# Kernel tuning notes

Hardware: AMD Instinct MI355X
Metric: run time of the kernel (lower is better)

## Reference

```python
import jax, jax.numpy as jnp
import numpy as np

HIDDEN = 2048
NUM_HEADS = 16
HEAD_DIM = 128
ROPE_BASE = 10000.0
B, L = 2, 2048


def _rotate_half(x):
    x1, x2 = jnp.split(x, 2, axis=-1)
    return jnp.concatenate((-x2, x1), axis=-1)


def _apply_rope(x, position_ids, base=ROPE_BASE):
    # x: [B, L, H, D]; position_ids: [L] (broadcast over batch)
    D = x.shape[-1]
    dim_idx = jnp.arange(0, D, 2, dtype=jnp.float32)
    inv_freq = 1.0 / (base ** (dim_idx / D))                      # [D/2]
    freqs = position_ids.astype(jnp.float32)[None, :, None] * inv_freq  # [1, L, D/2]
    # NOTE: faithful to source: sin/cos are repeat_interleaved ([s0,s0,s1,s1,...])
    sin = jnp.repeat(jnp.sin(freqs), 2, axis=-1)[:, :, None, :]   # [1, L, 1, D]
    cos = jnp.repeat(jnp.cos(freqs), 2, axis=-1)[:, :, None, :]
    return cos * x + _rotate_half(x) * sin


def setup_inputs() -> dict:
    key = jax.random.key(0)
    k1, k2, k3, k4, k5 = jax.random.split(key, 5)
    hidden_states = jax.random.normal(k1, (B, L, HIDDEN), dtype=jnp.float32)
    # causal additive mask, broadcastable over heads
    causal = jnp.tril(jnp.ones((L, L), dtype=bool))
    attention_mask = jnp.where(causal, 0.0, -1e9).astype(jnp.float32)
    attention_mask = jnp.broadcast_to(attention_mask, (B, 1, L, L))
    position_ids = jnp.arange(L, dtype=jnp.int64)
    s = 1.0 / np.sqrt(HIDDEN)
    Wq = jax.random.normal(k2, (HIDDEN, NUM_HEADS * HEAD_DIM), dtype=jnp.float32) * s
    Wk = jax.random.normal(k3, (HIDDEN, NUM_HEADS * HEAD_DIM), dtype=jnp.float32) * s
    Wv = jax.random.normal(k4, (HIDDEN, NUM_HEADS * HEAD_DIM), dtype=jnp.float32) * s
    Wo = jax.random.normal(k5, (NUM_HEADS * HEAD_DIM, HIDDEN), dtype=jnp.float32) * s
    return {"hidden_states": hidden_states, "attention_mask": attention_mask,
            "position_ids": position_ids, "Wq": Wq, "Wk": Wk, "Wv": Wv, "Wo": Wo}


def reference(hidden_states, attention_mask, position_ids, Wq, Wk, Wv, Wo):
    Bb, Ll, _ = hidden_states.shape
    H, D = NUM_HEADS, HEAD_DIM
    scale = D ** -0.5
    q = (hidden_states @ Wq).reshape(Bb, Ll, H, D)
    k = (hidden_states @ Wk).reshape(Bb, Ll, H, D)
    v = (hidden_states @ Wv).reshape(Bb, Ll, H, D)
    q = _apply_rope(q, position_ids)
    k = _apply_rope(k, position_ids)
    # [B, H, Lq, Lk]
    scores = jnp.einsum('bqhd,bkhd->bhqk', q, k) * scale + attention_mask
    attn = jax.nn.softmax(scores.astype(jnp.float32), axis=-1).astype(q.dtype)
    out = jnp.einsum('bhqk,bkhd->bqhd', attn, v).reshape(Bb, Ll, H * D)
    return out @ Wo
```

## Files before the change

kernel.cpp:

```cpp
#include <hip/hip_runtime.h>
#include <stdint.h>

typedef uint16_t u16;
typedef __attribute__((ext_vector_type(4))) float f32x4;
typedef __attribute__((ext_vector_type(4))) unsigned short u16x4;
typedef __attribute__((ext_vector_type(8))) __bf16 bf16x8;

#define HIDDEN 2048
#define LSEQ   2048
#define NH     16
#define HD     128
#define NQK    6144
#define QSCALE 0.12751743f
#define M0 32.0f

__device__ __forceinline__ u16 f2b(float f) {
  union { float f; uint32_t u; } v; v.f = f;
  uint32_t r = v.u + 0x7fffu + ((v.u >> 16) & 1u);
  return (u16)(r >> 16);
}
__device__ __forceinline__ float b2f(u16 h) {
  union { uint32_t u; float f; } v; v.u = ((uint32_t)h) << 16;
  return v.f;
}

__device__ __forceinline__ void gload16(const void* g, void* l) {
  __builtin_amdgcn_global_load_lds((const __attribute__((address_space(1))) void*)g,
                                   (__attribute__((address_space(3))) void*)l, 16, 0, 0);
}
__device__ __forceinline__ f32x4 mfma16(bf16x8 a, bf16x8 b, f32x4 c) {
  return __builtin_amdgcn_mfma_f32_16x16x32_bf16(a, b, c, 0, 0, 0);
}

__global__ void k_f32_to_bf16(const float* __restrict__ in, u16* __restrict__ out, int n4) {
  int i = blockIdx.x * 256 + threadIdx.x;
  if (i >= n4) return;
  float4 v = ((const float4*)in)[i];
  u16x4 o = { f2b(v.x), f2b(v.y), f2b(v.z), f2b(v.w) };
  ((u16x4*)out)[i] = o;
}

__global__ __launch_bounds__(256) void k_transpose_bf16(const float* __restrict__ W,
                                                        u16* __restrict__ WT, int R, int C,
                                                        float scale, int perm) {
  __shared__ u16 tile[64][65];
  const int bx = blockIdx.x, by = blockIdx.y;
  const int t = threadIdx.x;
  const int g = t >> 4, k = t & 15;
#pragma unroll
  for (int p = 0; p < 4; ++p) {
    int r = by * 64 + p * 16 + g;
    int c = bx * 64 + k * 4;
    float4 v = *(const float4*)(W + (size_t)r * C + c);
    tile[p * 16 + g][k * 4 + 0] = f2b(v.x * scale);
    tile[p * 16 + g][k * 4 + 1] = f2b(v.y * scale);
    tile[p * 16 + g][k * 4 + 2] = f2b(v.z * scale);
    tile[p * 16 + g][k * 4 + 3] = f2b(v.w * scale);
  }
  __syncthreads();
#pragma unroll
  for (int p = 0; p < 4; ++p) {
    int n = bx * 64 + p * 16 + g;
    if (perm) n = (n & ~127) | ((n & 63) << 1) | ((n >> 6) & 1);
    int kk = by * 64 + k * 4;
    u16x4 o = { tile[k * 4 + 0][p * 16 + g], tile[k * 4 + 1][p * 16 + g],
                tile[k * 4 + 2][p * 16 + g], tile[k * 4 + 3][p * 16 + g] };
    *(u16x4*)(WT + (size_t)n * R + kk) = o;
  }
}

__global__ __launch_bounds__(256) void k_transpose_v(const u16* __restrict__ qkv,
                                                     u16* __restrict__ vt) {
  __shared__ u16 tile[64][65];
  const int lt = blockIdx.x;
  const int dt = blockIdx.y;
  const int bh = blockIdx.z;
  const int t = threadIdx.x;
  const int g = t >> 4, k = t & 15;
  const u16* src = qkv + (size_t)(bh >> 4) * LSEQ * NQK + 2 * HIDDEN + (bh & 15) * HD;
#pragma unroll
  for (int p = 0; p < 4; ++p) {
    int l = lt * 64 + p * 16 + g;
    int d = dt * 64 + k * 4;
    u16x4 v = *(const u16x4*)(src + (size_t)l * NQK + d);
    tile[p * 16 + g][k * 4 + 0] = v[0];
    tile[p * 16 + g][k * 4 + 1] = v[1];
    tile[p * 16 + g][k * 4 + 2] = v[2];
    tile[p * 16 + g][k * 4 + 3] = v[3];
  }
  __syncthreads();
  u16* dst = vt + (size_t)bh * HD * LSEQ;
#pragma unroll
  for (int p = 0; p < 4; ++p) {
    int d = dt * 64 + p * 16 + g;
    int l = lt * 64 + k * 4;
    u16x4 o = { tile[k * 4 + 0][p * 16 + g], tile[k * 4 + 1][p * 16 + g],
                tile[k * 4 + 2][p * 16 + g], tile[k * 4 + 3][p * 16 + g] };
    *(u16x4*)(dst + (size_t)d * LSEQ + l) = o;
  }
}

__global__ void k_rope_table(const int* __restrict__ pos, float* __restrict__ tab, int pstride) {
  int i = blockIdx.x * 256 + threadIdx.x;
  int l = i >> 6, j = i & 63;
  float p = (float)pos[(size_t)l * pstride];
  float th = p * expf(-(float)j * 0.14391156642178528f);
  tab[2 * i + 0] = cosf(th);
  tab[2 * i + 1] = sinf(th);
}

template<int BF16OUT, int DOROPE>
__global__ __launch_bounds__(512, 2) void k_gemm2(const u16* __restrict__ A,
                                                  const u16* __restrict__ Bt,
                                                  void* __restrict__ Cv,
                                                  const float* __restrict__ tab,
                                                  int M, int N, int K) {
  __shared__ __align__(16) char lds[147456];
  const int tid = threadIdx.x, w = tid >> 6, lane = tid & 63;
  const int l15 = lane & 15, l4 = lane >> 4;
  const int wm = w >> 2, wn = w & 3;
  const int nbn = gridDim.x, nbm = gridDim.y;
  const int id = blockIdx.y * nbn + blockIdx.x;
  const int x = id & 7, k = id >> 3;
  const int g = nbm >> 3;
  const int bm = x * g + (k % g);
  const int bn = k / g;
  const u16* Ag = A + (size_t)bm * 128 * K;
  const u16* Bg = Bt + (size_t)bn * 256 * K;
  const int r7 = (tid >> 3) & 7;
  const int sw0 = ((0 + l4) ^ (l15 & 7)) * 16;
  const int sw1 = ((4 + l4) ^ (l15 & 7)) * 16;

  auto stageA = [&](int kt, int buf) {
    char* dst = lds + buf * 16384;
    const int k0 = kt << 6;
#pragma unroll
    for (int i = 0; i < 2; ++i) {
      int c = i * 512 + tid;
      int row = c >> 3, s = (c & 7) ^ r7;
      gload16(Ag + (size_t)row * K + k0 + s * 8, dst + (i * 512 + w * 64) * 16);
    }
  };
  auto stageBh = [&](int kt, int buf, int half) {
    char* dst = lds + 49152 + buf * 32768;
    const int k0 = kt << 6;
#pragma unroll
    for (int i = 0; i < 2; ++i) {
      int c = half * 1024 + i * 512 + tid;
      int row = c >> 3, s = (c & 7) ^ r7;
      gload16(Bg + (size_t)row * K + k0 + s * 8, dst + (half * 1024 + i * 512 + w * 64) * 16);
    }
  };

  const int NT = K >> 6;
  stageA(0, 0); stageBh(0, 0, 0); stageBh(0, 0, 1);
  stageA(1, 1); stageBh(1, 1, 0); stageBh(1, 1, 1);
  asm volatile("s_waitcnt vmcnt(6)" ::: "memory");
  __builtin_amdgcn_s_barrier();
  asm volatile("" ::: "memory");

  f32x4 acc[4][4] = {};
  int buf = 0, sbuf = 2;
  for (int t = 0; t < NT; ++t) {
    const char* Ab = lds + buf * 16384;
    const char* Bb = lds + 49152 + buf * 32768;
    const bool doStage = (t + 2 < NT);
    bf16x8 af[4][2], bfr[4][2];
    auto rdA = [&](int mi, int ks) {
      return *(const bf16x8*)(Ab + ((wm * 64 + mi * 16 + l15) << 7) + (ks ? sw1 : sw0));
    };
    auto rdB = [&](int nj, int ks) {
      return *(const bf16x8*)(Bb + ((wn * 64 + nj * 16 + l15) << 7) + (ks ? sw1 : sw0));
    };

#pragma unroll
    for (int mi = 0; mi < 2; ++mi) { af[mi][0] = rdA(mi, 0); af[mi][1] = rdA(mi, 1); }
#pragma unroll
    for (int nj = 0; nj < 2; ++nj) { bfr[nj][0] = rdB(nj, 0); bfr[nj][1] = rdB(nj, 1); }
    if (doStage) stageA(t + 2, sbuf);
    __builtin_amdgcn_s_setprio(1);
#pragma unroll
    for (int mi = 0; mi < 2; ++mi)
#pragma unroll
      for (int nj = 0; nj < 2; ++nj) {
        acc[mi][nj] = mfma16(af[mi][0], bfr[nj][0], acc[mi][nj]);
        acc[mi][nj] = mfma16(af[mi][1], bfr[nj][1], acc[mi][nj]);
      }
    __builtin_amdgcn_s_setprio(0);

#pragma unroll
    for (int nj = 2; nj < 4; ++nj) { bfr[nj][0] = rdB(nj, 0); bfr[nj][1] = rdB(nj, 1); }
    if (doStage) stageBh(t + 2, sbuf, 0);
    __builtin_amdgcn_s_setprio(1);
#pragma unroll
    for (int mi = 0; mi < 2; ++mi)
#pragma unroll
      for (int nj = 2; nj < 4; ++nj) {
        acc[mi][nj] = mfma16(af[mi][0], bfr[nj][0], acc[mi][nj]);
        acc[mi][nj] = mfma16(af[mi][1], bfr[nj][1], acc[mi][nj]);
      }
    __builtin_amdgcn_s_setprio(0);

#pragma unroll
    for (int mi = 2; mi < 4; ++mi) { af[mi][0] = rdA(mi, 0); af[mi][1] = rdA(mi, 1); }
    if (doStage) stageBh(t + 2, sbuf, 1);
    __builtin_amdgcn_s_setprio(1);
#pragma unroll
    for (int mi = 2; mi < 4; ++mi)
#pragma unroll
      for (int nj = 2; nj < 4; ++nj) {
        acc[mi][nj] = mfma16(af[mi][0], bfr[nj][0], acc[mi][nj]);
        acc[mi][nj] = mfma16(af[mi][1], bfr[nj][1], acc[mi][nj]);
      }
    __builtin_amdgcn_s_setprio(0);

    __builtin_amdgcn_s_setprio(1);
#pragma unroll
    for (int mi = 2; mi < 4; ++mi)
#pragma unroll
      for (int nj = 0; nj < 2; ++nj) {
        acc[mi][nj] = mfma16(af[mi][0], bfr[nj][0], acc[mi][nj]);
        acc[mi][nj] = mfma16(af[mi][1], bfr[nj][1], acc[mi][nj]);
      }
    __builtin_amdgcn_s_setprio(0);

    if (doStage) asm volatile("s_waitcnt vmcnt(6)" ::: "memory");
    else         asm volatile("s_waitcnt vmcnt(0)" ::: "memory");
    __builtin_amdgcn_s_barrier();
    asm volatile("" ::: "memory");
    buf = (buf == 2) ? 0 : buf + 1;
    sbuf = (sbuf == 2) ? 0 : sbuf + 1;
  }

  const float2* tb = (const float2*)tab;
#pragma unroll
  for (int mi = 0; mi < 4; ++mi) {
#pragma unroll
    for (int nj = 0; nj < 4; ++nj) {
      int row0 = bm * 128 + wm * 64 + mi * 16 + l4 * 4;
      int col  = bn * 256 + wn * 64 + nj * 16 + l15;
#pragma unroll
      for (int r = 0; r < 4; ++r) {
        float v = acc[mi][nj][r];
        if (DOROPE) {
          float vp = __shfl_xor(v, 1);
          if (col < 4096) {
            int l = (row0 + r) & (LSEQ - 1);
            float2 tt = tb[l * 64 + ((col & 127) >> 2) + ((l15 & 1) << 5)];
            v = (l15 & 1) ? (tt.x * v + tt.y * vp) : (tt.x * v - tt.y * vp);
          }
        }
        if (BF16OUT) ((u16*)Cv)[(size_t)(row0 + r) * N + col] = f2b(v);
        else         ((float*)Cv)[(size_t)(row0 + r) * N + col] = v;
      }
    }
  }
}

__global__ __launch_bounds__(512, 2) void k_attn(const u16* __restrict__ qkv,
                                                 const u16* __restrict__ vt,
                                                 u16* __restrict__ aout) {
  __shared__ __align__(16) u16 Ks[3][64 * 128];
  __shared__ __align__(16) u16 Vs[3][128 * 64];
  __shared__ __align__(16) u16 Ps[2][8 * 16 * 72];
  const int bid = blockIdx.x;
  const int bh = bid & 31, pairi = bid >> 5;
  const int b = bh >> 4, h = bh & 15;
  const int qtA = pairi, qtB = 15 - pairi;
  const int tid = threadIdx.x, w = tid >> 6, lane = tid & 63;
  const int l15 = lane & 15, l4 = lane >> 4;

  bf16x8 qfA[4], qfB[4];
  {
    const u16* qpA = qkv + (size_t)(b * LSEQ + qtA * 128 + w * 16 + l15) * NQK + h * HD;
    const u16* qpB = qkv + (size_t)(b * LSEQ + qtB * 128 + w * 16 + l15) * NQK + h * HD;
#pragma unroll
    for (int ks = 0; ks < 4; ++ks) {
      qfA[ks] = *(const bf16x8*)(qpA + ks * 32 + l4 * 8);
      qfB[ks] = *(const bf16x8*)(qpB + ks * 32 + l4 * 8);
    }
  }

  f32x4 accA[8] = {}, accB[8] = {};
  float mA[4], lA[4], mB[4], lB[4];
#pragma unroll
  for (int r = 0; r < 4; ++r) { mA[r] = M0; lA[r] = 0.f; mB[r] = M0; lB[r] = 0.f; }

  const u16* kb  = qkv + (size_t)b * LSEQ * NQK + HIDDEN + h * HD;
  const u16* vtb = vt + (size_t)bh * HD * LSEQ;
  const int ntA = 2 * qtA + 2, ntB = 2 * qtB + 2;
  const int qbaseA = qtA * 128 + w * 16, qbaseB = qtB * 128 + w * 16;

  auto stage = [&](int t, int bf) {
    const int kv0 = t * 64;
    char* Kd = (char*)(&Ks[bf][0]);
    char* Vd = (char*)(&Vs[bf][0]);
#pragma unroll
    for (int p = 0; p < 2; ++p) {
      int cc = p * 512 + tid;
      int row = cc >> 4, sl = cc & 15;
      gload16(kb + (size_t)(kv0 + row) * NQK + ((sl ^ (row & 7)) * 8), Kd + (p * 512 + w * 64) * 16);
    }
#pragma unroll
    for (int p = 0; p < 2; ++p) {
      int cc = p * 512 + tid;
      int d = cc >> 3, sl = cc & 7;
      gload16(vtb + (size_t)d * LSEQ + kv0 + ((sl ^ (d & 7)) * 8), Vd + (p * 512 + w * 64) * 16);
    }
  };

  auto tileCompute = [&](const bf16x8 (&qf)[4], f32x4 (&acc_o)[8], float (&mrun)[4],
                         float (&lrun)[4], int qbase, int kv0,
                         const char* KsC, const char* VsC, u16* ps) {
    f32x4 s4[4] = {};
    __builtin_amdgcn_s_setprio(1);
#pragma unroll
    for (int ks = 0; ks < 4; ++ks) {
#pragma unroll
      for (int nj = 0; nj < 4; ++nj) {
        int row = nj * 16 + l15;
        int co = (ks * 64 + l4 * 16) ^ ((row & 7) << 4);
        bf16x8 kf = *(const bf16x8*)(KsC + row * 256 + co);
        s4[nj] = mfma16(qf[ks], kf, s4[nj]);
      }
    }
    __builtin_amdgcn_s_setprio(0);

    const int qrow0 = qbase + l4 * 4;
    float pv[4][4], lm[4];
    if (kv0 + 63 <= qbase) {
#pragma unroll
      for (int r = 0; r < 4; ++r) {
        lm[r] = fmaxf(fmaxf(s4[0][r], s4[1][r]), fmaxf(s4[2][r], s4[3][r]));
#pragma unroll
        for (int nj = 0; nj < 4; ++nj) pv[nj][r] = s4[nj][r];
      }
    } else {
#pragma unroll
      for (int r = 0; r < 4; ++r) {
        float mx = -3e38f;
#pragma unroll
        for (int nj = 0; nj < 4; ++nj) {
          int kvcol = kv0 + nj * 16 + l15;
          float sv = (kvcol <= qrow0 + r) ? s4[nj][r] : -3e38f;
          pv[nj][r] = sv;
          mx = fmaxf(mx, sv);
        }
        lm[r] = mx;
      }
    }
    int over = (lm[0] > mrun[0]) | (lm[1] > mrun[1]) | (lm[2] > mrun[2]) | (lm[3] > mrun[3]);
    if (__builtin_expect(__any(over), 0)) {
#pragma unroll
      for (int r = 0; r < 4; ++r) {
        float px = lm[r];
        px = fmaxf(px, __shfl_xor(px, 1));
        px = fmaxf(px, __shfl_xor(px, 2));
        px = fmaxf(px, __shfl_xor(px, 4));
        px = fmaxf(px, __shfl_xor(px, 8));
        if (px > mrun[r]) {
          float cf = exp2f(mrun[r] - px);
          mrun[r] = px;
          lrun[r] *= cf;
#pragma unroll
          for (int df = 0; df < 8; ++df) acc_o[df][r] *= cf;
        }
      }
    }
#pragma unroll
    for (int r = 0; r < 4; ++r) {
      float s = 0.f;
#pragma unroll
      for (int nj = 0; nj < 4; ++nj) {
        float e = exp2f(pv[nj][r] - mrun[r]);
        pv[nj][r] = e;
        s += e;
      }
      lrun[r] += s;
    }
#pragma unroll
    for (int nj = 0; nj < 4; ++nj)
#pragma unroll
      for (int r = 0; r < 4; ++r)
        ps[(w * 16 + l4 * 4 + r) * 72 + nj * 16 + l15] = f2b(pv[nj][r]);

    bf16x8 pa[2];
#pragma unroll
    for (int ks2 = 0; ks2 < 2; ++ks2)
      pa[ks2] = *(const bf16x8*)(ps + (w * 16 + l15) * 72 + ks2 * 32 + l4 * 8);
    __builtin_amdgcn_s_setprio(1);
#pragma unroll
    for (int df = 0; df < 8; ++df) {
#pragma unroll
      for (int ks2 = 0; ks2 < 2; ++ks2) {
        int vrow = df * 16 + l15;
        int co = (ks2 * 64 + l4 * 16) ^ ((vrow & 7) << 4);
        bf16x8 bv = *(const bf16x8*)(VsC + vrow * 128 + co);
        acc_o[df] = mfma16(pa[ks2], bv, acc_o[df]);
      }
    }
    __builtin_amdgcn_s_setprio(0);
  };

  stage(0, 0);
  stage(1, 1);
  asm volatile("s_waitcnt vmcnt(4)" ::: "memory");
  __builtin_amdgcn_s_barrier();

  int buf = 0, sbuf = 2;
  for (int t = 0; t < ntB; ++t) {
    const bool doStage = (t + 2 < ntB);
    if (doStage) stage(t + 2, sbuf);
    const int kv0 = t * 64;
    const char* KsC = (const char*)(&Ks[buf][0]);
    const char* VsC = (const char*)(&Vs[buf][0]);

    if ((t < ntA) && (kv0 <= qbaseA + 15))
      tileCompute(qfA, accA, mA, lA, qbaseA, kv0, KsC, VsC, &Ps[0][0]);
    if (kv0 <= qbaseB + 15)
      tileCompute(qfB, accB, mB, lB, qbaseB, kv0, KsC, VsC, &Ps[1][0]);

    if (doStage) asm volatile("s_waitcnt vmcnt(4)" ::: "memory");
    else         asm volatile("s_waitcnt vmcnt(0)" ::: "memory");
    __builtin_amdgcn_s_barrier();
    buf = (buf == 2) ? 0 : buf + 1;
    sbuf = (sbuf == 2) ? 0 : sbuf + 1;
  }

#pragma unroll
  for (int r = 0; r < 4; ++r) {
    float sA = lA[r];
    sA += __shfl_xor(sA, 1); sA += __shfl_xor(sA, 2);
    sA += __shfl_xor(sA, 4); sA += __shfl_xor(sA, 8);
    float sB = lB[r];
    sB += __shfl_xor(sB, 1); sB += __shfl_xor(sB, 2);
    sB += __shfl_xor(sB, 4); sB += __shfl_xor(sB, 8);
    float invA = 1.f / sA;
    float invB = 1.f / sB;
    u16* opA = aout + (size_t)(b * LSEQ + qtA * 128 + w * 16 + l4 * 4 + r) * HIDDEN + h * HD;
    u16* opB = aout + (size_t)(b * LSEQ + qtB * 128 + w * 16 + l4 * 4 + r) * HIDDEN + h * HD;
#pragma unroll
    for (int df = 0; df < 8; ++df) {
      opA[df * 16 + l15] = f2b(accA[df][r] * invA);
      opB[df * 16 + l15] = f2b(accB[df][r] * invB);
    }
  }
}

extern "C" void kernel_launch(void* const* d_in, const int* in_sizes, int n_in,
                              void* d_out, int out_size, void* d_ws, size_t ws_size,
                              hipStream_t stream) {
  const float* hidden = (const float*)d_in[0];
  const int*   pos = (const int*)d_in[2];
  const float* Wq = (const float*)d_in[3];
  const float* Wk = (const float*)d_in[4];
  const float* Wv = (const float*)d_in[5];
  const float* Wo = (const float*)d_in[6];
  float* out = (float*)d_out;

  char* ws = (char*)d_ws;
  u16* hbf   = (u16*)ws;
  u16* WT    = (u16*)(ws + 16777216);
  u16* vt    = WT;
  u16* WoT   = (u16*)(ws + 16777216 + 25165824);
  u16* qkv   = (u16*)(ws + 50331648);
  float* tab = (float*)(ws + 100663296);
  u16* aout  = hbf;

  int pstride = (in_sizes[2] == LSEQ) ? 1 : 2;

  k_f32_to_bf16<<<8192, 256, 0, stream>>>(hidden, hbf, 2097152);
  dim3 tg(32, 32);
  k_transpose_bf16<<<tg, 256, 0, stream>>>(Wq, WT,                   2048, 2048, QSCALE, 1);
  k_transpose_bf16<<<tg, 256, 0, stream>>>(Wk, WT + 2048 * 2048,     2048, 2048, 1.0f, 1);
  k_transpose_bf16<<<tg, 256, 0, stream>>>(Wv, WT + 2 * 2048 * 2048, 2048, 2048, 1.0f, 0);
  k_transpose_bf16<<<tg, 256, 0, stream>>>(Wo, WoT,                  2048, 2048, 1.0f, 0);
  k_rope_table<<<512, 256, 0, stream>>>(pos, tab, pstride);
  k_gemm2<1, 1><<<dim3(24, 32), 512, 0, stream>>>(hbf, WT, qkv, tab, 4096, 6144, 2048);
  k_transpose_v<<<dim3(32, 2, 32), 256, 0, stream>>>(qkv, vt);
  k_attn<<<256, 512, 0, stream>>>(qkv, vt, aout);
  k_gemm2<0, 0><<<dim3(8, 32), 512, 0, stream>>>(aout, WoT, out, nullptr, 4096, 2048, 2048);
}
```

Measured before the change: 279.9 us.

## Merge weight transposes and rope table into one prep launch; remap GEMM tile order

The four weight transpose/convert launches and the rope-table launch are combined into a single kernel with a z-dimension selecting the job, removing four launch gaps and letting the jobs run concurrently. The GEMM block-to-tile mapping also changes: workgroups are reordered by XCD (id&7) into a contiguous linear tile index with n varying fastest, which changes L2 locality per XCD. The fused kernel adds branching per block, and the z==4 slice launches 1024 blocks where only 512 do work.

```diff
diff --git a/kernel.cpp b/kernel.cpp
--- a/kernel.cpp
+++ b/kernel.cpp
@@ -19,10 +19,6 @@
   uint32_t r = v.u + 0x7fffu + ((v.u >> 16) & 1u);
   return (u16)(r >> 16);
 }
-__device__ __forceinline__ float b2f(u16 h) {
-  union { uint32_t u; float f; } v; v.u = ((uint32_t)h) << 16;
-  return v.f;
-}
 
 __device__ __forceinline__ void gload16(const void* g, void* l) {
   __builtin_amdgcn_global_load_lds((const __attribute__((address_space(1))) void*)g,
@@ -40,9 +36,30 @@
   ((u16x4*)out)[i] = o;
 }
 
-__global__ __launch_bounds__(256) void k_transpose_bf16(const float* __restrict__ W,
-                                                        u16* __restrict__ WT, int R, int C,
-                                                        float scale, int perm) {
+__global__ __launch_bounds__(256) void k_prep(const float* __restrict__ Wq,
+                                              const float* __restrict__ Wk,
+                                              const float* __restrict__ Wv,
+                                              const float* __restrict__ Wo,
+                                              u16* __restrict__ WT, u16* __restrict__ WoT,
+                                              const int* __restrict__ pos, int pstride,
+                                              float* __restrict__ tab) {
+  const int z = blockIdx.z;
+  if (z == 4) {
+    int i = (blockIdx.y * 32 + blockIdx.x) * 256 + threadIdx.x;
+    if (i >= LSEQ * 64) return;
+    int l = i >> 6, j = i & 63;
+    float p = (float)pos[(size_t)l * pstride];
+    float th = p * expf(-(float)j * 0.14391156642178528f);
+    tab[2 * i + 0] = cosf(th);
+    tab[2 * i + 1] = sinf(th);
+    return;
+  }
+  const float* W = (z == 0) ? Wq : (z == 1) ? Wk : (z == 2) ? Wv : Wo;
+  u16* D = (z < 3) ? (WT + (size_t)z * HIDDEN * HIDDEN) : WoT;
+  const float scale = (z == 0) ? QSCALE : 1.0f;
+  const int perm = (z < 2);
+  const int R = HIDDEN, C = HIDDEN;
+
   __shared__ u16 tile[64][65];
   const int bx = blockIdx.x, by = blockIdx.y;
   const int t = threadIdx.x;
@@ -65,7 +82,7 @@
     int kk = by * 64 + k * 4;
     u16x4 o = { tile[k * 4 + 0][p * 16 + g], tile[k * 4 + 1][p * 16 + g],
                 tile[k * 4 + 2][p * 16 + g], tile[k * 4 + 3][p * 16 + g] };
-    *(u16x4*)(WT + (size_t)n * R + kk) = o;
+    *(u16x4*)(D + (size_t)n * R + kk) = o;
   }
 }
 
@@ -98,15 +115,6 @@
                 tile[k * 4 + 2][p * 16 + g], tile[k * 4 + 3][p * 16 + g] };
     *(u16x4*)(dst + (size_t)d * LSEQ + l) = o;
   }
-}
-
-__global__ void k_rope_table(const int* __restrict__ pos, float* __restrict__ tab, int pstride) {
-  int i = blockIdx.x * 256 + threadIdx.x;
-  int l = i >> 6, j = i & 63;
-  float p = (float)pos[(size_t)l * pstride];
-  float th = p * expf(-(float)j * 0.14391156642178528f);
-  tab[2 * i + 0] = cosf(th);
-  tab[2 * i + 1] = sinf(th);
 }
 
 template<int BF16OUT, int DOROPE>
@@ -119,12 +127,12 @@
   const int tid = threadIdx.x, w = tid >> 6, lane = tid & 63;
   const int l15 = lane & 15, l4 = lane >> 4;
   const int wm = w >> 2, wn = w & 3;
-  const int nbn = gridDim.x, nbm = gridDim.y;
-  const int id = blockIdx.y * nbn + blockIdx.x;
-  const int x = id & 7, k = id >> 3;
-  const int g = nbm >> 3;
-  const int bm = x * g + (k % g);
-  const int bn = k / g;
+  const int nbx = gridDim.x;
+  const int nwg = nbx * gridDim.y;
+  const int id = blockIdx.y * nbx + blockIdx.x;
+  const int qq = nwg >> 3;
+  const int sid = (id & 7) * qq + (id >> 3);
+  const int bn = sid % nbx, bm = sid / nbx;
   const u16* Ag = A + (size_t)bm * 128 * K;
   const u16* Bg = Bt + (size_t)bn * 256 * K;
   const int r7 = (tid >> 3) & 7;
@@ -470,12 +478,7 @@
   int pstride = (in_sizes[2] == LSEQ) ? 1 : 2;
 
   k_f32_to_bf16<<<8192, 256, 0, stream>>>(hidden, hbf, 2097152);
-  dim3 tg(32, 32);
-  k_transpose_bf16<<<tg, 256, 0, stream>>>(Wq, WT,                   2048, 2048, QSCALE, 1);
-  k_transpose_bf16<<<tg, 256, 0, stream>>>(Wk, WT + 2048 * 2048,     2048, 2048, 1.0f, 1);
-  k_transpose_bf16<<<tg, 256, 0, stream>>>(Wv, WT + 2 * 2048 * 2048, 2048, 2048, 1.0f, 0);
-  k_transpose_bf16<<<tg, 256, 0, stream>>>(Wo, WoT,                  2048, 2048, 1.0f, 0);
-  k_rope_table<<<512, 256, 0, stream>>>(pos, tab, pstride);
+  k_prep<<<dim3(32, 32, 5), 256, 0, stream>>>(Wq, Wk, Wv, Wo, WT, WoT, pos, pstride, tab);
   k_gemm2<1, 1><<<dim3(24, 32), 512, 0, stream>>>(hbf, WT, qkv, tab, 4096, 6144, 2048);
   k_transpose_v<<<dim3(32, 2, 32), 256, 0, stream>>>(qkv, vt);
   k_attn<<<256, 512, 0, stream>>>(qkv, vt, aout);
```

Measured after the change: 293.5 us. 4.9% more time.
